# Performance work log

Measured on AMD Instinct MI355X. Metric: run time of the kernel, lower is better.

Reference implementation:

```python
import jax, jax.numpy as jnp
import numpy as np

B, N, P, S = 8, 4096, 16, 200
W_SPS, W_EXT, W_CUB, W_CD = 0.1, 0.1, 1.0, 1.0
EXIST_THRED = 24.0

# cube face constants (from Loss._init_buffers)
MASK_PROJECT = jnp.array([[0,1,1],[0,1,1],[1,0,1],[1,0,1],[1,1,0],[1,1,0]], jnp.float32)  # [6,3]
MASK_PLANE   = jnp.array([[1,0,0],[1,0,0],[0,1,0],[0,1,0],[0,0,1],[0,0,1]], jnp.float32)  # [6,3]
CUBE_NORMAL  = jnp.array([[-1,0,0],[1,0,0],[0,-1,0],[0,1,0],[0,0,-1],[0,0,1]], jnp.float32)  # [6,3]
CUBE_PLANES6 = jnp.tile(jnp.array([[-1.,-1.,-1.],[1.,1.,1.]], jnp.float32), (3,1))  # [6,3] rows -,+,-,+,-,+


def setup_inputs() -> dict:
    key = jax.random.key(0)
    ks = jax.random.split(key, 10)
    pc = jax.random.normal(ks[0], (B, N, 3), jnp.float32)
    normals = jax.random.normal(ks[1], (B, N, 3), jnp.float32)
    normals = normals / jnp.linalg.norm(normals, axis=-1, keepdims=True)
    trans = 0.1 * jax.random.normal(ks[2], (B, P, 3), jnp.float32)
    Q, _ = jnp.linalg.qr(jax.random.normal(ks[3], (B, P, 3, 3), jnp.float32))
    rotate = Q  # random orthonormal rotation-like matrices
    scale = jax.random.uniform(ks[4], (B, P, 3), jnp.float32, 0.1, 1.0)
    shape_eps = jax.random.uniform(ks[5], (B, P, 2), jnp.float32, 0.2, 1.8)
    exist = jax.random.uniform(ks[6], (B, P, 1), jnp.float32, 0.01, 0.99)
    aw = jax.random.uniform(ks[7], (B, N, P), jnp.float32)
    assign_matrix = aw / aw.sum(-1, keepdims=True)
    etas = jax.random.uniform(ks[8], (B, P, S), jnp.float32, -1.47, 1.47)
    omegas = jax.random.uniform(ks[9], (B, P, S), jnp.float32, -3.1, 3.1)
    return dict(pc=pc, normals=normals, trans=trans, rotate=rotate, scale=scale,
                shape_eps=shape_eps, exist=exist, assign_matrix=assign_matrix,
                etas=etas, omegas=omegas)


def transform_to_primitive_frame(x, trans, rotate):
    # x: [B,N,3], trans: [B,P,3], rotate: [B,P,3,3] -> R^T (x - t): [B,P,N,3]
    d = x[:, None, :, :] - trans[:, :, None, :]
    return jnp.einsum('bpji,bpnj->bpni', rotate, d)


def fexp(x, p):
    return jnp.sign(x) * jnp.abs(x) ** p


def sample_sq_points(scale, eps, etas, omegas):
    # scale [B,P,3], eps [B,P,2], etas/omegas [B,P,S] -> points [B,P,S,3]
    etas = jnp.where(etas == 0, etas + 1e-6, etas)
    omegas = jnp.where(omegas == 0, omegas + 1e-6, omegas)
    a1, a2, a3 = scale[..., 0:1], scale[..., 1:2], scale[..., 2:3]
    e1, e2 = eps[..., 0:1], eps[..., 1:2]
    ce, se = jnp.cos(etas), jnp.sin(etas)
    co, so = jnp.cos(omegas), jnp.sin(omegas)
    x = a1 * fexp(ce, e1) * fexp(co, e2)
    y = a2 * fexp(ce, e1) * fexp(so, e2)
    z = a3 * fexp(se, e1)
    clamp = lambda v: ((v > 0).astype(v.dtype) * 2 - 1) * jnp.maximum(jnp.abs(v), 1e-6)
    return jnp.stack([clamp(x), clamp(y), clamp(z)], -1)


def compute_cuboid_loss(pc_inver, normals_inver, scale, assign_matrix):
    pcN = jnp.transpose(pc_inver, (0, 2, 1, 3))       # [B,N,P,3]
    nN = jnp.transpose(normals_inver, (0, 2, 1, 3))   # [B,N,P,3]
    # cosine similarity against 6 unit face normals (eps=1e-4 clamp)
    nrm = jnp.maximum(jnp.linalg.norm(nN, axis=-1, keepdims=True), 1e-4)
    sim = jnp.einsum('bnpd,fd->bnpf', nN, CUBE_NORMAL) / nrm  # [B,N,P,6]
    idx = jnp.argmax(sim, axis=-1)                    # [B,N,P]
    s = scale[:, None, :, None, :]                    # [B,1,P,1,3]
    planes_scaled = CUBE_PLANES6[None, None, None] * s  # [B,1,P,6,3]
    pcp = pcN[:, :, :, None, :] * MASK_PROJECT + planes_scaled * MASK_PLANE  # [B,N,P,6,3]
    pcp = jnp.clip(pcp, -s, s)
    b, n, p = pcp.shape[:3]
    gidx = jnp.broadcast_to(idx[..., None, None], (b, n, p, 1, 3))
    proj = jnp.take_along_axis(pcp, gidx, axis=3)[:, :, :, 0, :]  # [B,N,P,3]
    diff = ((proj - pcN) ** 2).sum(-1)                # [B,N,P]
    return jnp.mean((diff * assign_matrix).sum(-1))


def compute_cd_loss(pc_inver, scale, shape_eps, etas, omegas, assign_matrix, exist):
    X = sample_sq_points(scale, shape_eps, etas, omegas)  # [B,P,S,3]
    # squared pairwise distances D[b,p,s,n] via ||x||^2+||y||^2-2xy
    D = ((X ** 2).sum(-1)[..., None]
         + (pc_inver ** 2).sum(-1)[:, :, None, :]
         - 2.0 * jnp.einsum('bpsd,bpnd->bpsn', X, pc_inver))
    D = jnp.maximum(D, 0.0)
    pcl_to_prim = D.min(axis=2)                       # [B,P,N]
    pcl_to_prim_loss = jnp.mean((jnp.transpose(pcl_to_prim, (0, 2, 1)) * assign_matrix).sum(-1))
    # original returns (pcl_to_prim_loss, pcl_to_prim_loss)
    return pcl_to_prim_loss, pcl_to_prim_loss


def compute_existence_loss(assign_matrix, exist):
    gt = jax.lax.stop_gradient((assign_matrix.sum(1) > EXIST_THRED).astype(jnp.float32))  # [B,P]
    p = exist[..., 0]
    bce = -(gt * jnp.maximum(jnp.log(p), -100.0) + (1.0 - gt) * jnp.maximum(jnp.log(1.0 - p), -100.0))
    return jnp.mean(bce)


def get_sparsity_loss(assign_matrix):
    num_points = assign_matrix.shape[1]
    norm_05 = jnp.sqrt(assign_matrix.sum(1) / num_points + 0.01).mean(1) ** 2  # [B]
    return jnp.mean(norm_05)


def reference(pc, normals, trans, rotate, scale, shape_eps, exist, assign_matrix, etas, omegas):
    etas = jax.lax.stop_gradient(etas)      # sampler output is detached in original
    omegas = jax.lax.stop_gradient(omegas)
    pc_inver = transform_to_primitive_frame(pc, trans, rotate)       # [B,P,N,3]
    normals_inver = transform_to_primitive_frame(normals, trans, rotate)
    cub = compute_cuboid_loss(pc_inver, normals_inver, scale, assign_matrix)
    p2p, prim2p = compute_cd_loss(pc_inver, scale, shape_eps, etas, omegas, assign_matrix, exist)
    cd = p2p + prim2p
    ext = compute_existence_loss(assign_matrix, exist)
    sps = get_sparsity_loss(assign_matrix)
    return W_CUB * cub + W_CD * cd + W_EXT * ext + W_SPS * sps
```

## Files before the change

### kernel.cpp

```cpp
#include <hip/hip_runtime.h>
#include <math.h>

#define BB 8
#define NN 4096
#define PP 16
#define SS 200

#define X_FLOATS (BB*PP*SS*4)
#define ZERO_FLOATS (2 + BB*PP)

__global__ void sq_points_kernel(const float* __restrict__ scale,
                                 const float* __restrict__ shape_eps,
                                 const float* __restrict__ etas,
                                 const float* __restrict__ omegas,
                                 float4* __restrict__ X,
                                 float* __restrict__ zero_region) {
    int idx = blockIdx.x * blockDim.x + threadIdx.x;
    if (blockIdx.x == 0 && threadIdx.x < ZERO_FLOATS) zero_region[threadIdx.x] = 0.f;
    if (idx >= BB * PP * SS) return;
    int bp = idx / SS;
    float eta = etas[idx];
    float om  = omegas[idx];
    if (eta == 0.f) eta = 1e-6f;
    if (om  == 0.f) om  = 1e-6f;
    float a1 = scale[bp*3+0], a2 = scale[bp*3+1], a3 = scale[bp*3+2];
    float e1 = shape_eps[bp*2+0], e2 = shape_eps[bp*2+1];
    float ce = cosf(eta), se = sinf(eta);
    float co = cosf(om),  so = sinf(om);
    auto fexp = [](float x, float p) {
        float sg = (x > 0.f) ? 1.f : ((x < 0.f) ? -1.f : 0.f);
        return sg * powf(fabsf(x), p);
    };
    float fce = fexp(ce, e1);
    float x = a1 * fce * fexp(co, e2);
    float y = a2 * fce * fexp(so, e2);
    float z = a3 * fexp(se, e1);
    auto clampv = [](float v) {
        return ((v > 0.f) ? 1.f : -1.f) * fmaxf(fabsf(v), 1e-6f);
    };
    x = clampv(x); y = clampv(y); z = clampv(z);
    float xsq = x*x + y*y + z*z;
    X[idx] = make_float4(-2.f*x, -2.f*y, -2.f*z, xsq);
}

__global__ __launch_bounds__(256) void main_kernel(
    const float* __restrict__ pc, const float* __restrict__ normals,
    const float* __restrict__ trans, const float* __restrict__ rotate,
    const float* __restrict__ scale, const float* __restrict__ assign,
    const float4* __restrict__ Xd, float* __restrict__ accum,
    float* __restrict__ colsum) {
    __shared__ float4 Xs[SS];
    __shared__ float rc[4], rd[4], ra[4];

    int blk = blockIdx.x;
    int chunk = blk & 3;
    int p = (blk >> 2) & 15;
    int b = blk >> 6;
    int bp = b * PP + p;

    const float4* __restrict__ Xp = Xd + (size_t)bp * SS;
    if (threadIdx.x < SS) Xs[threadIdx.x] = Xp[threadIdx.x];

    float tx = trans[bp*3+0], ty = trans[bp*3+1], tz = trans[bp*3+2];
    float R0 = rotate[bp*9+0], R1 = rotate[bp*9+1], R2 = rotate[bp*9+2];
    float R3 = rotate[bp*9+3], R4 = rotate[bp*9+4], R5 = rotate[bp*9+5];
    float R6 = rotate[bp*9+6], R7 = rotate[bp*9+7], R8 = rotate[bp*9+8];
    float sx = scale[bp*3+0], sy = scale[bp*3+1], sz = scale[bp*3+2];

    float y0[4], y1[4], y2[4], ysq[4], aw[4];
    float acc_cub = 0.f, acc_as = 0.f;
#pragma unroll
    for (int j = 0; j < 4; j++) {
        int n = chunk * 1024 + j * 256 + threadIdx.x;
        size_t base = ((size_t)b * NN + n) * 3;
        float px = pc[base+0], py = pc[base+1], pz = pc[base+2];
        float qx = normals[base+0], qy = normals[base+1], qz = normals[base+2];
        aw[j] = assign[((size_t)b * NN + n) * PP + p];

        float d0 = px - tx, d1 = py - ty, d2 = pz - tz;
        y0[j] = R0*d0 + R3*d1 + R6*d2;
        y1[j] = R1*d0 + R4*d1 + R7*d2;
        y2[j] = R2*d0 + R5*d1 + R8*d2;
        float e0 = qx - tx, e1 = qy - ty, e2 = qz - tz;
        float m0 = R0*e0 + R3*e1 + R6*e2;
        float m1 = R1*e0 + R4*e1 + R7*e2;
        float m2 = R2*e0 + R5*e1 + R8*e2;

        float rn = 1.f / fmaxf(sqrtf(m0*m0 + m1*m1 + m2*m2), 1e-4f);
        float s0 = -m0*rn, s1 = m0*rn, s2 = -m1*rn, s3 = m1*rn, s4 = -m2*rn, s5 = m2*rn;
        int fidx = 0; float best = s0;
        if (s1 > best) { best = s1; fidx = 1; }
        if (s2 > best) { best = s2; fidx = 2; }
        if (s3 > best) { best = s3; fidx = 3; }
        if (s4 > best) { best = s4; fidx = 4; }
        if (s5 > best) { best = s5; fidx = 5; }
        int axis = fidx >> 1;
        float sgn = (fidx & 1) ? 1.f : -1.f;
        float pjx = fminf(fmaxf(y0[j], -sx), sx);
        float pjy = fminf(fmaxf(y1[j], -sy), sy);
        float pjz = fminf(fmaxf(y2[j], -sz), sz);
        if (axis == 0)      pjx = sgn * sx;
        else if (axis == 1) pjy = sgn * sy;
        else                pjz = sgn * sz;
        float dxx = pjx - y0[j], dyy = pjy - y1[j], dzz = pjz - y2[j];
        acc_cub += (dxx*dxx + dyy*dyy + dzz*dzz) * aw[j];
        ysq[j] = y0[j]*y0[j] + y1[j]*y1[j] + y2[j]*y2[j];
        acc_as += aw[j];
    }

    __syncthreads();

    float mmA[4] = {1e30f, 1e30f, 1e30f, 1e30f};
    float mmB[4] = {1e30f, 1e30f, 1e30f, 1e30f};
#pragma unroll 2
    for (int s = 0; s < SS; s += 2) {
        float4 xa = Xs[s+0], xb = Xs[s+1];
#pragma unroll
        for (int j = 0; j < 4; j++) {
            mmA[j] = fminf(mmA[j], fmaf(xa.x, y0[j], fmaf(xa.y, y1[j], fmaf(xa.z, y2[j], xa.w))));
            mmB[j] = fminf(mmB[j], fmaf(xb.x, y0[j], fmaf(xb.y, y1[j], fmaf(xb.z, y2[j], xb.w))));
        }
    }
    float acc_cd = 0.f;
#pragma unroll
    for (int j = 0; j < 4; j++) {
        float mn = fminf(mmA[j], mmB[j]);
        acc_cd += fmaxf(mn + ysq[j], 0.f) * aw[j];
    }

#pragma unroll
    for (int off = 32; off > 0; off >>= 1) {
        acc_cub += __shfl_down(acc_cub, off, 64);
        acc_cd  += __shfl_down(acc_cd,  off, 64);
        acc_as  += __shfl_down(acc_as,  off, 64);
    }
    int wave = threadIdx.x >> 6, lane = threadIdx.x & 63;
    if (lane == 0) { rc[wave] = acc_cub; rd[wave] = acc_cd; ra[wave] = acc_as; }
    __syncthreads();
    if (threadIdx.x == 0) {
        atomicAdd(&accum[0], rc[0]+rc[1]+rc[2]+rc[3]);
        atomicAdd(&accum[1], rd[0]+rd[1]+rd[2]+rd[3]);
        atomicAdd(&colsum[bp], ra[0]+ra[1]+ra[2]+ra[3]);
    }
}

__global__ void finalize_kernel(const float* __restrict__ exist,
                                const float* __restrict__ colsum,
                                const float* __restrict__ accum,
                                float* __restrict__ out) {
    int t = threadIdx.x;
    __shared__ float bce_s[128], sq_s[128];
    float cs = colsum[t];
    float gt = (cs > 24.0f) ? 1.f : 0.f;
    float pe = exist[t];
    float lg  = fmaxf(logf(pe), -100.f);
    float lg1 = fmaxf(logf(1.f - pe), -100.f);
    bce_s[t] = -(gt * lg + (1.f - gt) * lg1);
    sq_s[t] = sqrtf(cs / (float)NN + 0.01f);
    __syncthreads();
    if (t == 0) {
        float ext = 0.f;
        for (int i = 0; i < 128; i++) ext += bce_s[i];
        ext /= 128.f;
        float sps = 0.f;
        for (int b = 0; b < 8; b++) {
            float mb = 0.f;
            for (int p = 0; p < 16; p++) mb += sq_s[b*16 + p];
            mb /= 16.f;
            sps += mb * mb;
        }
        sps /= 8.f;
        float cub = accum[0] / (float)(BB * NN);
        float p2p = accum[1] / (float)(BB * NN);
        float cd  = 2.f * p2p;
        out[0] = 1.0f * cub + 1.0f * cd + 0.1f * ext + 0.1f * sps;
    }
}

extern "C" void kernel_launch(void* const* d_in, const int* in_sizes, int n_in,
                              void* d_out, int out_size, void* d_ws, size_t ws_size,
                              hipStream_t stream) {
    const float* pc        = (const float*)d_in[0];
    const float* normals   = (const float*)d_in[1];
    const float* trans     = (const float*)d_in[2];
    const float* rotate    = (const float*)d_in[3];
    const float* scale     = (const float*)d_in[4];
    const float* shape_eps = (const float*)d_in[5];
    const float* exist     = (const float*)d_in[6];
    const float* assign    = (const float*)d_in[7];
    const float* etas      = (const float*)d_in[8];
    const float* omegas    = (const float*)d_in[9];

    float* ws = (float*)d_ws;
    float4* X = (float4*)ws;
    float* accum  = ws + X_FLOATS;
    float* colsum = accum + 2;

    sq_points_kernel<<<(BB*PP*SS + 255)/256, 256, 0, stream>>>(
        scale, shape_eps, etas, omegas, X, accum );
    main_kernel<<<BB*PP*4, 256, 0, stream>>>(
        pc, normals, trans, rotate, scale, assign, X, accum, colsum);
    finalize_kernel<<<1, 128, 0, stream>>>(exist, colsum, accum, (float*)d_out);
}
```

Measured before the change: 102.1 us.

## Fuse superquadric sampling into main kernel and replace atomics with per-block partials

Each main-kernel block now computes its own primitive's 200 superquadric sample points straight into shared memory, so the separate sampling kernel, its global buffer round-trip and one launch go away. Global atomics are replaced by per-block partial sums that a widened 256-thread finalize kernel reduces, which also removes the need for a zeroing pass. The inner min loop's unroll factor rises from 2 to 4. The cost is that the trig and pow work is repeated across the 4 chunk blocks of each primitive.

```diff
diff --git a/kernel.cpp b/kernel.cpp
--- a/kernel.cpp
+++ b/kernel.cpp
@@ -5,61 +5,52 @@
 #define NN 4096
 #define PP 16
 #define SS 200
-
-#define X_FLOATS (BB*PP*SS*4)
-#define ZERO_FLOATS (2 + BB*PP)
-
-__global__ void sq_points_kernel(const float* __restrict__ scale,
-                                 const float* __restrict__ shape_eps,
-                                 const float* __restrict__ etas,
-                                 const float* __restrict__ omegas,
-                                 float4* __restrict__ X,
-                                 float* __restrict__ zero_region) {
-    int idx = blockIdx.x * blockDim.x + threadIdx.x;
-    if (blockIdx.x == 0 && threadIdx.x < ZERO_FLOATS) zero_region[threadIdx.x] = 0.f;
-    if (idx >= BB * PP * SS) return;
-    int bp = idx / SS;
-    float eta = etas[idx];
-    float om  = omegas[idx];
-    if (eta == 0.f) eta = 1e-6f;
-    if (om  == 0.f) om  = 1e-6f;
-    float a1 = scale[bp*3+0], a2 = scale[bp*3+1], a3 = scale[bp*3+2];
-    float e1 = shape_eps[bp*2+0], e2 = shape_eps[bp*2+1];
-    float ce = cosf(eta), se = sinf(eta);
-    float co = cosf(om),  so = sinf(om);
-    auto fexp = [](float x, float p) {
-        float sg = (x > 0.f) ? 1.f : ((x < 0.f) ? -1.f : 0.f);
-        return sg * powf(fabsf(x), p);
-    };
-    float fce = fexp(ce, e1);
-    float x = a1 * fce * fexp(co, e2);
-    float y = a2 * fce * fexp(so, e2);
-    float z = a3 * fexp(se, e1);
-    auto clampv = [](float v) {
-        return ((v > 0.f) ? 1.f : -1.f) * fmaxf(fabsf(v), 1e-6f);
-    };
-    x = clampv(x); y = clampv(y); z = clampv(z);
-    float xsq = x*x + y*y + z*z;
-    X[idx] = make_float4(-2.f*x, -2.f*y, -2.f*z, xsq);
-}
+#define NCHUNK 4
+#define NBLK (BB*PP*NCHUNK)
+
 
 __global__ __launch_bounds__(256) void main_kernel(
     const float* __restrict__ pc, const float* __restrict__ normals,
     const float* __restrict__ trans, const float* __restrict__ rotate,
-    const float* __restrict__ scale, const float* __restrict__ assign,
-    const float4* __restrict__ Xd, float* __restrict__ accum,
-    float* __restrict__ colsum) {
+    const float* __restrict__ scale, const float* __restrict__ shape_eps,
+    const float* __restrict__ assign,
+    const float* __restrict__ etas, const float* __restrict__ omegas,
+    float* __restrict__ cub_part, float* __restrict__ cd_part,
+    float* __restrict__ colsum_part) {
     __shared__ float4 Xs[SS];
     __shared__ float rc[4], rd[4], ra[4];
 
     int blk = blockIdx.x;
-    int chunk = blk & 3;
-    int p = (blk >> 2) & 15;
-    int b = blk >> 6;
-    int bp = b * PP + p;
-
-    const float4* __restrict__ Xp = Xd + (size_t)bp * SS;
-    if (threadIdx.x < SS) Xs[threadIdx.x] = Xp[threadIdx.x];
+    int chunk = blk & (NCHUNK-1);
+    int bp = blk >> 2;
+    int b = bp >> 4;
+    int p = bp & 15;
+
+    if (threadIdx.x < SS) {
+        int idx = bp * SS + threadIdx.x;
+        float eta = etas[idx];
+        float om  = omegas[idx];
+        if (eta == 0.f) eta = 1e-6f;
+        if (om  == 0.f) om  = 1e-6f;
+        float a1 = scale[bp*3+0], a2 = scale[bp*3+1], a3 = scale[bp*3+2];
+        float e1 = shape_eps[bp*2+0], e2 = shape_eps[bp*2+1];
+        float ce = cosf(eta), se = sinf(eta);
+        float co = cosf(om),  so = sinf(om);
+        auto fexp = [](float x, float pw) {
+            float sg = (x > 0.f) ? 1.f : ((x < 0.f) ? -1.f : 0.f);
+            return sg * powf(fabsf(x), pw);
+        };
+        float fce = fexp(ce, e1);
+        float x = a1 * fce * fexp(co, e2);
+        float y = a2 * fce * fexp(so, e2);
+        float z = a3 * fexp(se, e1);
+        auto clampv = [](float v) {
+            return ((v > 0.f) ? 1.f : -1.f) * fmaxf(fabsf(v), 1e-6f);
+        };
+        x = clampv(x); y = clampv(y); z = clampv(z);
+        float xsq = x*x + y*y + z*z;
+        Xs[threadIdx.x] = make_float4(-2.f*x, -2.f*y, -2.f*z, xsq);
+    }
 
     float tx = trans[bp*3+0], ty = trans[bp*3+1], tz = trans[bp*3+2];
     float R0 = rotate[bp*9+0], R1 = rotate[bp*9+1], R2 = rotate[bp*9+2];
@@ -112,7 +103,7 @@
 
     float mmA[4] = {1e30f, 1e30f, 1e30f, 1e30f};
     float mmB[4] = {1e30f, 1e30f, 1e30f, 1e30f};
-#pragma unroll 2
+#pragma unroll 4
     for (int s = 0; s < SS; s += 2) {
         float4 xa = Xs[s+0], xb = Xs[s+1];
 #pragma unroll
@@ -138,40 +129,55 @@
     if (lane == 0) { rc[wave] = acc_cub; rd[wave] = acc_cd; ra[wave] = acc_as; }
     __syncthreads();
     if (threadIdx.x == 0) {
-        atomicAdd(&accum[0], rc[0]+rc[1]+rc[2]+rc[3]);
-        atomicAdd(&accum[1], rd[0]+rd[1]+rd[2]+rd[3]);
-        atomicAdd(&colsum[bp], ra[0]+ra[1]+ra[2]+ra[3]);
+        cub_part[blk]    = rc[0]+rc[1]+rc[2]+rc[3];
+        cd_part[blk]     = rd[0]+rd[1]+rd[2]+rd[3];
+        colsum_part[blk] = ra[0]+ra[1]+ra[2]+ra[3];
     }
 }
 
 __global__ void finalize_kernel(const float* __restrict__ exist,
-                                const float* __restrict__ colsum,
-                                const float* __restrict__ accum,
+                                const float* __restrict__ cub_part,
+                                const float* __restrict__ cd_part,
+                                const float* __restrict__ colsum_part,
                                 float* __restrict__ out) {
     int t = threadIdx.x;
-    __shared__ float bce_s[128], sq_s[128];
-    float cs = colsum[t];
-    float gt = (cs > 24.0f) ? 1.f : 0.f;
-    float pe = exist[t];
-    float lg  = fmaxf(logf(pe), -100.f);
-    float lg1 = fmaxf(logf(1.f - pe), -100.f);
-    bce_s[t] = -(gt * lg + (1.f - gt) * lg1);
-    sq_s[t] = sqrtf(cs / (float)NN + 0.01f);
+    __shared__ float bce_s[128], sq_s[128], rcub[4], rcd[4];
+
+    float c1 = cub_part[t] + cub_part[t + 256];
+    float c2 = cd_part[t]  + cd_part[t + 256];
+#pragma unroll
+    for (int off = 32; off > 0; off >>= 1) {
+        c1 += __shfl_down(c1, off, 64);
+        c2 += __shfl_down(c2, off, 64);
+    }
+    int wave = t >> 6, lane = t & 63;
+    if (lane == 0) { rcub[wave] = c1; rcd[wave] = c2; }
+
+    if (t < 128) {
+        float cs = colsum_part[t*4+0] + colsum_part[t*4+1]
+                 + colsum_part[t*4+2] + colsum_part[t*4+3];
+        float gt = (cs > 24.0f) ? 1.f : 0.f;
+        float pe = exist[t];
+        float lg  = fmaxf(logf(pe), -100.f);
+        float lg1 = fmaxf(logf(1.f - pe), -100.f);
+        bce_s[t] = -(gt * lg + (1.f - gt) * lg1);
+        sq_s[t] = sqrtf(cs / (float)NN + 0.01f);
+    }
     __syncthreads();
     if (t == 0) {
         float ext = 0.f;
         for (int i = 0; i < 128; i++) ext += bce_s[i];
         ext /= 128.f;
         float sps = 0.f;
-        for (int b = 0; b < 8; b++) {
+        for (int bb = 0; bb < 8; bb++) {
             float mb = 0.f;
-            for (int p = 0; p < 16; p++) mb += sq_s[b*16 + p];
+            for (int pp2 = 0; pp2 < 16; pp2++) mb += sq_s[bb*16 + pp2];
             mb /= 16.f;
             sps += mb * mb;
         }
         sps /= 8.f;
-        float cub = accum[0] / (float)(BB * NN);
-        float p2p = accum[1] / (float)(BB * NN);
+        float cub = (rcub[0]+rcub[1]+rcub[2]+rcub[3]) / (float)(BB * NN);
+        float p2p = (rcd[0]+rcd[1]+rcd[2]+rcd[3]) / (float)(BB * NN);
         float cd  = 2.f * p2p;
         out[0] = 1.0f * cub + 1.0f * cd + 0.1f * ext + 0.1f * sps;
     }
@@ -192,13 +198,13 @@
     const float* omegas    = (const float*)d_in[9];
 
     float* ws = (float*)d_ws;
-    float4* X = (float4*)ws;
-    float* accum  = ws + X_FLOATS;
-    float* colsum = accum + 2;
-
-    sq_points_kernel<<<(BB*PP*SS + 255)/256, 256, 0, stream>>>(
-        scale, shape_eps, etas, omegas, X, accum );
-    main_kernel<<<BB*PP*4, 256, 0, stream>>>(
-        pc, normals, trans, rotate, scale, assign, X, accum, colsum);
-    finalize_kernel<<<1, 128, 0, stream>>>(exist, colsum, accum, (float*)d_out);
+    float* cub_part    = ws;
+    float* cd_part     = ws + NBLK;
+    float* colsum_part = ws + 2*NBLK;
+
+    main_kernel<<<NBLK, 256, 0, stream>>>(
+        pc, normals, trans, rotate, scale, shape_eps, assign, etas, omegas,
+        cub_part, cd_part, colsum_part);
+    finalize_kernel<<<1, 256, 0, stream>>>(
+        exist, cub_part, cd_part, colsum_part, (float*)d_out);
 }
```

Result: faster. 89.18 us (-12.7%).
